# Kernel optimization log

Hardware: AMD Instinct MI355X
Metric: run time of the kernel (lower is better)

Reference implementation:

```python
import jax, jax.numpy as jnp
import numpy as np

EPS = 1e-5  # BatchNorm eps (torch default)


def _coords():
    # coord_tensor[i] = [(i//5 - 2)/2, (i%5 - 2)/2] for 5x5 grid of 25 objects
    i = jnp.arange(25)
    return jnp.stack([(i // 5 - 2) / 2.0, (i % 5 - 2) / 2.0], axis=-1).astype(jnp.float32)


def _conv_bn(x, w, b, gamma, beta):
    # conv stride2 pad1 -> relu -> batchnorm (training-mode batch stats, as torch module default)
    y = jax.lax.conv_general_dilated(x, w, (2, 2), ((1, 1), (1, 1)),
                                     dimension_numbers=('NCHW', 'OIHW', 'NCHW'))
    y = jax.nn.relu(y + b[None, :, None, None])
    m = y.mean(axis=(0, 2, 3), keepdims=True)
    v = y.var(axis=(0, 2, 3), keepdims=True)
    return gamma[None, :, None, None] * (y - m) * jax.lax.rsqrt(v + EPS) + beta[None, :, None, None]


def setup_inputs() -> dict:
    key = jax.random.key(0)
    ks = iter(jax.random.split(key, 64))
    def rn(shape, scale=0.05):
        return jax.random.normal(next(ks), shape, jnp.float32) * scale
    B = 256
    inp = {
        'x': jax.random.normal(next(ks), (B, 3, 80, 80), jnp.float32),
        'qst': jax.random.normal(next(ks), (B, 11), jnp.float32),
    }
    for l, (ci, co) in enumerate([(3, 24), (24, 24), (24, 24), (24, 24)], 1):
        inp[f'cw{l}'] = rn((co, ci, 3, 3))
        inp[f'cb{l}'] = jnp.zeros((co,), jnp.float32)
        inp[f'bg{l}'] = jnp.ones((co,), jnp.float32)
        inp[f'bb{l}'] = jnp.zeros((co,), jnp.float32)
    for l, (di, do) in enumerate([(63, 256), (256, 256), (256, 256), (256, 256)], 1):
        inp[f'gw{l}'] = rn((di, do))
        inp[f'gb{l}'] = jnp.zeros((do,), jnp.float32)
    for l, (di, do) in enumerate([(256, 256), (256, 256), (256, 10)], 1):
        inp[f'fw{l}'] = rn((di, do))
        inp[f'fb{l}'] = jnp.zeros((do,), jnp.float32)
    return inp


def _forward(x, qst, cw1, cb1, bg1, bb1, cw2, cb2, bg2, bb2,
             cw3, cb3, bg3, bb3, cw4, cb4, bg4, bb4,
             gw1, gb1, gw2, gb2, gw3, gb3, gw4, gb4,
             fw1, fb1, fw2, fb2, fw3, fb3):
    B = x.shape[0]
    # Convolution stack: (B,3,80,80) -> (B,24,5,5)
    h = _conv_bn(x, cw1, cb1, bg1, bb1)
    h = _conv_bn(h, cw2, cb2, bg2, bb2)
    h = _conv_bn(h, cw3, cb3, bg3, bb3)
    h = _conv_bn(h, cw4, cb4, bg4, bb4)
    # Objects: (B,24,25) -> (B,25,24) -> concat coords -> (B,25,26)
    obj = h.reshape(B, 24, 25).transpose(0, 2, 1)
    obj = jnp.concatenate([obj, jnp.broadcast_to(_coords()[None], (B, 25, 2))], axis=-1)
    # Pairwise broadcast-concat: cat([x_i, x_j, qst]) with x_i[b,p,q]=obj[b,q], x_j[b,p,q]=obj[b,p]
    xi = jnp.broadcast_to(obj[:, None, :, :], (B, 25, 25, 26))
    xj = jnp.broadcast_to(obj[:, :, None, :], (B, 25, 25, 26))
    qb = jnp.broadcast_to(qst[:, None, None, :], (B, 25, 25, 11))
    pairs = jnp.concatenate([xi, xj, qb], axis=-1).reshape(B, 625, 63)
    g = jax.nn.relu(pairs @ gw1 + gb1)
    g = jax.nn.relu(g @ gw2 + gb2)
    g = jax.nn.relu(g @ gw3 + gb3)
    g = jax.nn.relu(g @ gw4 + gb4).sum(axis=1)  # (B,256)
    # f_phi (dropout treated as identity for a deterministic reference)
    f = jax.nn.relu(g @ fw1 + fb1)
    f = jax.nn.relu(f @ fw2 + fb2)
    logits = f @ fw3 + fb3
    return jax.nn.log_softmax(logits, axis=1)


def reference(x, qst, cw1, cb1, bg1, bb1, cw2, cb2, bg2, bb2,
              cw3, cb3, bg3, bb3, cw4, cb4, bg4, bb4,
              gw1, gb1, gw2, gb2, gw3, gb3, gw4, gb4,
              fw1, fb1, fw2, fb2, fw3, fb3):
    return _forward(x, qst, cw1, cb1, bg1, bb1, cw2, cb2, bg2, bb2,
                    cw3, cb3, bg3, bb3, cw4, cb4, bg4, bb4,
                    gw1, gb1, gw2, gb2, gw3, gb3, gw4, gb4,
                    fw1, fb1, fw2, fb2, fw3, fb3)
```

## Files before the change

kernel.cpp:

```cpp
#include <hip/hip_runtime.h>
#include <hip/hip_bf16.h>


typedef __attribute__((ext_vector_type(8))) short short8;
typedef __attribute__((ext_vector_type(4))) float floatx4;

__device__ __forceinline__ unsigned short f2bf(float v){
  union { float f; unsigned int u; } c; c.f = v;
  unsigned int u = c.u;
  u += 0x7FFFu + ((u >> 16) & 1u);
  return (unsigned short)(u >> 16);
}

__global__ __launch_bounds__(256) void prep_w_zero(
    const float* __restrict__ gw2, const float* __restrict__ gw3,
    const float* __restrict__ gw4, unsigned short* __restrict__ wf,
    float* __restrict__ stats)
{
  const int bid = blockIdx.x, tid = threadIdx.x;
  if (bid == 0){ for (int j = tid; j < 1536; j += 256) stats[j] = 0.f; }
  const int w = bid >> 8;
  const float* gw = (w == 0) ? gw2 : (w == 1) ? gw3 : gw4;
  const int idx = (bid & 255)*256 + tid;
  const int i = idx & 7, lane = (idx >> 3) & 63, t = (idx >> 9) & 15, kk = idx >> 13;
  const int k = kk*32 + (lane >> 4)*8 + i;
  const int c = t*16 + (lane & 15);
  wf[w*65536 + idx] = f2bf(gw[k*256 + c]);
}

template<int CI, int COG, int CIB>
__global__ __launch_bounds__(256) void conv_relu_stats(
    const float* __restrict__ in,
    const float* __restrict__ stats_in, const float* __restrict__ gprev,
    const float* __restrict__ bprev, float invN,
    const float* __restrict__ cw, const float* __restrict__ cb,
    float* __restrict__ out, float* __restrict__ stats_out,
    int H, int W, int OH, int OW)
{
  const int co0 = blockIdx.y * COG;
  __shared__ float ssm[2*CI];
  __shared__ float psum[4][COG], psum2[4][COG];
  const int tid = threadIdx.x;
  if (tid < CI){
    if (stats_in){
      float S = 0.f, S2 = 0.f;
      #pragma unroll
      for (int sh = 0; sh < 8; sh++){ S += stats_in[sh*48 + tid]; S2 += stats_in[sh*48 + 24 + tid]; }
      const float mean = S*invN;
      const float var  = S2*invN - mean*mean;
      const float rs   = rsqrtf(var + 1e-5f);
      const float sc   = gprev[tid]*rs;
      ssm[tid] = sc; ssm[CI + tid] = bprev[tid] - mean*sc;
    } else { ssm[tid] = 1.f; ssm[CI + tid] = 0.f; }
  }
  __syncthreads();
  const int idx = blockIdx.x*256 + tid;
  const int ow = idx % OW; const int t2 = idx / OW;
  const int oh = t2 % OH;  const int b  = t2 / OH;
  const float* cwb = cw + co0*CI*9;
  float accv[COG];
  #pragma unroll
  for (int g = 0; g < COG; g++) accv[g] = cb[co0 + g];
  for (int ci0 = 0; ci0 < CI; ci0 += CIB){
    float v[CIB*9];
    #pragma unroll
    for (int cj = 0; cj < CIB; cj++){
      const int ci = ci0 + cj;
      const float* ip = in + ((long)(b*CI + ci))*H*W;
      const float sc = ssm[ci], sh2 = ssm[CI + ci];
      #pragma unroll
      for (int kh = 0; kh < 3; kh++){
        const int ih = oh*2 - 1 + kh;
        const bool hok = (kh > 0) | (oh > 0);
        #pragma unroll
        for (int kw = 0; kw < 3; kw++){
          const int iw = ow*2 - 1 + kw;
          const bool ok = hok & ((kw > 0) | (ow > 0));
          const float raw = ip[ok ? ih*W + iw : 0];
          v[cj*9 + kh*3 + kw] = ok ? raw*sc + sh2 : 0.f;
        }
      }
    }
    #pragma unroll
    for (int cj = 0; cj < CIB; cj++)
      #pragma unroll
      for (int t = 0; t < 9; t++){
        const float vv = v[cj*9 + t];
        #pragma unroll
        for (int g = 0; g < COG; g++)
          accv[g] += vv * cwb[(g*CI + ci0 + cj)*9 + t];
      }
  }
  const int wave = tid >> 6, lane = tid & 63;
  #pragma unroll
  for (int g = 0; g < COG; g++){
    const float v2 = fmaxf(accv[g], 0.f);
    accv[g] = v2;
    out[(((long)b*24 + co0 + g)*OH + oh)*OW + ow] = v2;
  }
  #pragma unroll
  for (int g = 0; g < COG; g++){
    float s = accv[g], s2 = accv[g]*accv[g];
    for (int off = 32; off; off >>= 1){ s += __shfl_down(s, off); s2 += __shfl_down(s2, off); }
    if (lane == 0){ psum[wave][g] = s; psum2[wave][g] = s2; }
  }
  __syncthreads();
  if (tid < COG){
    const float S  = psum[0][tid] + psum[1][tid] + psum[2][tid] + psum[3][tid];
    const float S2 = psum2[0][tid] + psum2[1][tid] + psum2[2][tid] + psum2[3][tid];
    const int sh = blockIdx.x & 7;
    atomicAdd(&stats_out[sh*48 + co0 + tid],      S);
    atomicAdd(&stats_out[sh*48 + 24 + co0 + tid], S2);
  }
}

__global__ __launch_bounds__(512) void g_mega(
    const float* __restrict__ y4, const float* __restrict__ stats4,
    const float* __restrict__ bg4, const float* __restrict__ bb4,
    const float* __restrict__ qst, const float* __restrict__ gw1,
    const float* __restrict__ gb1,
    const unsigned short* __restrict__ Wf,
    const float* __restrict__ gb2, const float* __restrict__ gb3, const float* __restrict__ gb4,
    const float* __restrict__ fw1, const float* __restrict__ fb1,
    const float* __restrict__ fw2, const float* __restrict__ fb2,
    const float* __restrict__ fw3, const float* __restrict__ fb3,
    float* __restrict__ out)
{
  __shared__ __align__(16) short act[128*256];
  __shared__ __align__(16) float A_lds[25][260];
  __shared__ __align__(16) float Bm_lds[25][260];
  __shared__ float obj[25][26];
  __shared__ float ssum[48];
  __shared__ float ssm[48];
  __shared__ float scratch[512];
  __shared__ __align__(16) float bufA[256], bufB[256];
  __shared__ float lg[10];

  const int b = blockIdx.x, tid = threadIdx.x;
  char* actB = (char*)act;
  const int wave = tid >> 6, lane = tid & 63;
  const int lmod = lane & 15, ldiv = lane >> 4;
  const int wm = wave >> 2, wn = wave & 3;

  if (tid < 48){
    float S = 0.f;
    #pragma unroll
    for (int sh = 0; sh < 8; sh++) S += stats4[sh*48 + tid];
    ssum[tid] = S;
  }
  __syncthreads();
  if (tid < 24){
    const float mean = ssum[tid]*(1.f/6400.f);
    const float var  = ssum[24 + tid]*(1.f/6400.f) - mean*mean;
    const float rs   = rsqrtf(var + 1e-5f);
    const float sc   = bg4[tid]*rs;
    ssm[tid] = sc; ssm[24 + tid] = bb4[tid] - mean*sc;
  }
  __syncthreads();
  for (int j = tid; j < 600; j += 512){
    const int q = j/24, c = j%24;
    obj[q][c] = ssm[c]*y4[((long)(b*24 + c))*25 + q] + ssm[24 + c];
  }
  if (tid < 50){
    const int q = tid >> 1;
    obj[q][24 + (tid & 1)] = (tid & 1) ? (float)(q%5 - 2)*0.5f : (float)(q/5 - 2)*0.5f;
  }
  __syncthreads();
  {
    const int n = tid & 255, half = tid >> 8;
    float wa[26], wb[26];
    #pragma unroll
    for (int c = 0; c < 26; c++){ wa[c] = gw1[c*256 + n]; wb[c] = gw1[(26 + c)*256 + n]; }
    float qv = gb1[n];
    #pragma unroll
    for (int j = 0; j < 11; j++) qv += qst[b*11 + j]*gw1[(52 + j)*256 + n];
    const int q0 = half ? 13 : 0, q1 = half ? 25 : 13;
    for (int q = q0; q < q1; q++){
      float a = qv, bm = 0.f;
      #pragma unroll
      for (int c = 0; c < 26; c++){ const float o = obj[q][c]; a += o*wa[c]; bm += o*wb[c]; }
      A_lds[q][n] = a; Bm_lds[q][n] = bm;
    }
  }
  __syncthreads();

  float gsum = 0.f;
  for (int blk = 0; blk < 5; blk++){
    const int rowbase = blk * 128;
    const int nrows = min(128, 625 - rowbase);
    {
      const int r  = tid >> 2;
      const int q4 = tid & 3;
      if (r < nrows){
        const int row = rowbase + r;
        const float* ap = &A_lds [row % 25][q4*4];
        const float* bp = &Bm_lds[row / 25][q4*4];
        #pragma unroll
        for (int j = 0; j < 16; j++){
          const int c = j*16;
          floatx4 av = *(const floatx4*)(ap + c);
          floatx4 bv = *(const floatx4*)(bp + c);
          unsigned int p0 = (unsigned int)f2bf(fmaxf(av.x+bv.x, 0.f))
                          | ((unsigned int)f2bf(fmaxf(av.y+bv.y, 0.f)) << 16);
          unsigned int p1 = (unsigned int)f2bf(fmaxf(av.z+bv.z, 0.f))
                          | ((unsigned int)f2bf(fmaxf(av.w+bv.w, 0.f)) << 16);
          const int byte = (r*512 + (c + q4*4)*2) ^ ((r & 7) << 4);
          *(uint2*)(actB + byte) = make_uint2(p0, p1);
        }
      } else {
        #pragma unroll
        for (int j = 0; j < 16; j++){
          const int byte = (r*512 + (j*16 + q4*4)*2) ^ ((r & 7) << 4);
          *(uint2*)(actB + byte) = make_uint2(0u, 0u);
        }
      }
    }
    __syncthreads();

    for (int L = 0; L < 3; L++){
      floatx4 acc[4][4];
      #pragma unroll
      for (int m = 0; m < 4; m++)
        #pragma unroll
        for (int n = 0; n < 4; n++)
          acc[m][n] = (floatx4){0.f,0.f,0.f,0.f};
      const short8* wlayer = (const short8*)Wf + (long)L*8192;
      #pragma unroll
      for (int kk = 0; kk < 8; kk++){
        short8 bf[4];
        #pragma unroll
        for (int n = 0; n < 4; n++)
          bf[n] = wlayer[(kk*16 + wn*4 + n)*64 + lane];
        short8 af[4];
        #pragma unroll
        for (int m = 0; m < 4; m++){
          const int arow  = wm*64 + m*16 + lmod;
          const int abyte = (arow*512 + kk*64 + ldiv*16) ^ ((arow & 7) << 4);
          af[m] = *(const short8*)(actB + abyte);
        }
        #pragma unroll
        for (int n = 0; n < 4; n++)
          #pragma unroll
          for (int m = 0; m < 4; m++)
            acc[m][n] = __builtin_amdgcn_mfma_f32_16x16x32_bf16(af[m], bf[n], acc[m][n], 0, 0, 0);
      }

      if (L < 2){
        const float* bias = (L == 0) ? gb2 : gb3;
        __syncthreads();
        #pragma unroll
        for (int n = 0; n < 4; n++){
          const int c = (wn*4 + n)*16 + lmod;
          const float bv = bias[c];
          #pragma unroll
          for (int m = 0; m < 4; m++){
            #pragma unroll
            for (int i = 0; i < 4; i++){
              const int row = wm*64 + m*16 + ldiv*4 + i;
              const float v = fmaxf(acc[m][n][i] + bv, 0.f);
              const int byte = (row*512 + c*2) ^ ((row & 7) << 4);
              *(short*)(actB + byte) = (short)f2bf(v);
            }
          }
        }
        __syncthreads();
      } else {
        __syncthreads();
        #pragma unroll
        for (int n = 0; n < 4; n++){
          const int c = (wn*4 + n)*16 + lmod;
          const float bv = gb4[c];
          float sv = 0.f;
          #pragma unroll
          for (int m = 0; m < 4; m++){
            #pragma unroll
            for (int i = 0; i < 4; i++){
              const int row = wm*64 + m*16 + ldiv*4 + i;
              const float v = fmaxf(acc[m][n][i] + bv, 0.f);
              if (row < nrows) sv += v;
            }
          }
          sv += __shfl_xor(sv, 16);
          sv += __shfl_xor(sv, 32);
          if (ldiv == 0) scratch[wm*256 + c] = sv;
        }
        __syncthreads();
        if (tid < 256) gsum += scratch[tid] + scratch[256 + tid];
      }
    }
  }

  if (tid < 256) bufA[tid] = gsum;
  __syncthreads();
  const int n = tid & 255;
  float acc = 0.f;
  if (tid < 256){
    acc = fb1[n];
    const float4* pa = (const float4*)bufA;
    #pragma unroll 8
    for (int k4 = 0; k4 < 64; k4++){
      const float4 a = pa[k4];
      acc += a.x*fw1[(k4*4 + 0)*256 + n];
      acc += a.y*fw1[(k4*4 + 1)*256 + n];
      acc += a.z*fw1[(k4*4 + 2)*256 + n];
      acc += a.w*fw1[(k4*4 + 3)*256 + n];
    }
    bufB[n] = fmaxf(acc, 0.f);
  }
  __syncthreads();
  if (tid < 256){
    acc = fb2[n];
    const float4* pb = (const float4*)bufB;
    #pragma unroll 8
    for (int k4 = 0; k4 < 64; k4++){
      const float4 a = pb[k4];
      acc += a.x*fw2[(k4*4 + 0)*256 + n];
      acc += a.y*fw2[(k4*4 + 1)*256 + n];
      acc += a.z*fw2[(k4*4 + 2)*256 + n];
      acc += a.w*fw2[(k4*4 + 3)*256 + n];
    }
  }
  __syncthreads();
  if (tid < 256) bufA[n] = fmaxf(acc, 0.f);
  __syncthreads();
  if (tid < 10){
    float a3 = fb3[tid];
    for (int k = 0; k < 256; k++) a3 += bufA[k]*fw3[k*10 + tid];
    lg[tid] = a3;
  }
  __syncthreads();
  if (tid < 10){
    float m = lg[0];
    #pragma unroll
    for (int j = 1; j < 10; j++) m = fmaxf(m, lg[j]);
    float s = 0.f;
    #pragma unroll
    for (int j = 0; j < 10; j++) s += expf(lg[j] - m);
    out[b*10 + tid] = lg[tid] - m - logf(s);
  }
}

extern "C" void kernel_launch(void* const* d_in, const int* in_sizes, int n_in,
                              void* d_out, int out_size, void* d_ws, size_t ws_size,
                              hipStream_t stream)
{
  const float* x   = (const float*)d_in[0];
  const float* qst = (const float*)d_in[1];
  const float* cw1 = (const float*)d_in[2];
  const float* cb1 = (const float*)d_in[3];
  const float* bg1 = (const float*)d_in[4];
  const float* bb1 = (const float*)d_in[5];
  const float* cw2 = (const float*)d_in[6];
  const float* cb2 = (const float*)d_in[7];
  const float* bg2 = (const float*)d_in[8];
  const float* bb2 = (const float*)d_in[9];
  const float* cw3 = (const float*)d_in[10];
  const float* cb3 = (const float*)d_in[11];
  const float* bg3 = (const float*)d_in[12];
  const float* bb3 = (const float*)d_in[13];
  const float* cw4 = (const float*)d_in[14];
  const float* cb4 = (const float*)d_in[15];
  const float* bg4 = (const float*)d_in[16];
  const float* bb4 = (const float*)d_in[17];
  const float* gw1 = (const float*)d_in[18];
  const float* gb1 = (const float*)d_in[19];
  const float* gw2 = (const float*)d_in[20];
  const float* gb2 = (const float*)d_in[21];
  const float* gw3 = (const float*)d_in[22];
  const float* gb3 = (const float*)d_in[23];
  const float* gw4 = (const float*)d_in[24];
  const float* gb4 = (const float*)d_in[25];
  const float* fw1 = (const float*)d_in[26];
  const float* fb1 = (const float*)d_in[27];
  const float* fw2 = (const float*)d_in[28];
  const float* fb2 = (const float*)d_in[29];
  const float* fw3 = (const float*)d_in[30];
  const float* fb3 = (const float*)d_in[31];

  float* wsf    = (float*)d_ws;
  unsigned short* Wf = (unsigned short*)(wsf + 65728);
  float* stats  = wsf + 164032;
  float* y1     = wsf + 240832;
  float* y2     = wsf + 10071232;
  float* y3     = wsf + 12528832;
  float* y4     = wsf + 13143232;

  prep_w_zero<<<768, 256, 0, stream>>>(gw2, gw3, gw4, Wf, stats);
  conv_relu_stats<3,24,3><<<dim3(1600,1), 256, 0, stream>>>(x, nullptr, nullptr, nullptr, 0.f,
                                               cw1, cb1, y1, stats + 0, 80,80,40,40);
  conv_relu_stats<24,8,4><<<dim3(400,3), 256, 0, stream>>>(y1, stats + 0, bg1, bb1, 1.f/409600.f,
                                               cw2, cb2, y2, stats + 384, 40,40,20,20);
  conv_relu_stats<24,8,4><<<dim3(100,3), 256, 0, stream>>>(y2, stats + 384, bg2, bb2, 1.f/102400.f,
                                               cw3, cb3, y3, stats + 768, 20,20,10,10);
  conv_relu_stats<24,8,4><<<dim3(25,3), 256, 0, stream>>>(y3, stats + 768, bg3, bb3, 1.f/25600.f,
                                              cw4, cb4, y4, stats + 1152, 10,10,5,5);
  g_mega<<<256, 512, 0, stream>>>(y4, stats + 1152, bg4, bb4, qst, gw1, gb1, Wf,
                                  gb2, gb3, gb4, fw1, fb1, fw2, fb2, fw3, fb3,
                                  (float*)d_out);
}
```

Baseline: 286.7 us.

## Compute multiple output pixels per thread in conv kernels with shared input columns

Each conv thread now produces PX adjacent output pixels, loading one 3x(2PX+1) input window per channel so overlapping stride-2 columns are reused across the pixels. Outputs are written with float4/float2 stores and per-thread partial sums feed the batch-norm statistics reduction. Conv1 is split across three output-channel groups instead of one, and grid sizes shrink to match. The aim is fewer redundant global loads and address computations per output, at the cost of more registers per thread and fewer threads launched.

```diff
diff --git a/kernel.cpp b/kernel.cpp
--- a/kernel.cpp
+++ b/kernel.cpp
@@ -28,8 +28,8 @@
   wf[w*65536 + idx] = f2bf(gw[k*256 + c]);
 }
 
-template<int CI, int COG, int CIB>
-__global__ __launch_bounds__(256) void conv_relu_stats(
+template<int CI, int COG, int PX>
+__global__ __launch_bounds__(256) void conv_px(
     const float* __restrict__ in,
     const float* __restrict__ stats_in, const float* __restrict__ gprev,
     const float* __restrict__ bprev, float invN,
@@ -54,55 +54,71 @@
     } else { ssm[tid] = 1.f; ssm[CI + tid] = 0.f; }
   }
   __syncthreads();
+  const int nw = OW / PX;
   const int idx = blockIdx.x*256 + tid;
-  const int ow = idx % OW; const int t2 = idx / OW;
+  const int pw = idx % nw; const int t2 = idx / nw;
   const int oh = t2 % OH;  const int b  = t2 / OH;
+  const int ow0 = pw * PX;
   const float* cwb = cw + co0*CI*9;
-  float accv[COG];
+  constexpr int NC = 2*PX + 1;
+  float acc[PX][COG];
   #pragma unroll
-  for (int g = 0; g < COG; g++) accv[g] = cb[co0 + g];
-  for (int ci0 = 0; ci0 < CI; ci0 += CIB){
-    float v[CIB*9];
-    #pragma unroll
-    for (int cj = 0; cj < CIB; cj++){
-      const int ci = ci0 + cj;
-      const float* ip = in + ((long)(b*CI + ci))*H*W;
-      const float sc = ssm[ci], sh2 = ssm[CI + ci];
+  for (int j = 0; j < PX; j++)
+    #pragma unroll
+    for (int g = 0; g < COG; g++) acc[j][g] = cb[co0 + g];
+
+  #pragma unroll 1
+  for (int ci = 0; ci < CI; ci++){
+    const float* ip = in + ((long)(b*CI + ci))*H*W;
+    const float sc = ssm[ci], sh2 = ssm[CI + ci];
+    float v[3][NC];
+    #pragma unroll
+    for (int kh = 0; kh < 3; kh++){
+      const int ih = oh*2 - 1 + kh;
+      const bool hok = (ih >= 0);
+      #pragma unroll
+      for (int c9 = 0; c9 < NC; c9++){
+        const int iw = ow0*2 - 1 + c9;
+        const bool ok = hok & (iw >= 0);
+        const float raw = ip[ok ? ih*W + iw : 0];
+        v[kh][c9] = ok ? raw*sc + sh2 : 0.f;
+      }
+    }
+    #pragma unroll
+    for (int g = 0; g < COG; g++){
       #pragma unroll
       for (int kh = 0; kh < 3; kh++){
-        const int ih = oh*2 - 1 + kh;
-        const bool hok = (kh > 0) | (oh > 0);
-        #pragma unroll
-        for (int kw = 0; kw < 3; kw++){
-          const int iw = ow*2 - 1 + kw;
-          const bool ok = hok & ((kw > 0) | (ow > 0));
-          const float raw = ip[ok ? ih*W + iw : 0];
-          v[cj*9 + kh*3 + kw] = ok ? raw*sc + sh2 : 0.f;
-        }
+        const float w0 = cwb[(g*CI + ci)*9 + kh*3 + 0];
+        const float w1 = cwb[(g*CI + ci)*9 + kh*3 + 1];
+        const float w2 = cwb[(g*CI + ci)*9 + kh*3 + 2];
+        #pragma unroll
+        for (int j = 0; j < PX; j++)
+          acc[j][g] += v[kh][2*j]*w0 + v[kh][2*j+1]*w1 + v[kh][2*j+2]*w2;
       }
     }
-    #pragma unroll
-    for (int cj = 0; cj < CIB; cj++)
-      #pragma unroll
-      for (int t = 0; t < 9; t++){
-        const float vv = v[cj*9 + t];
-        #pragma unroll
-        for (int g = 0; g < COG; g++)
-          accv[g] += vv * cwb[(g*CI + ci0 + cj)*9 + t];
-      }
-  }
+  }
+
   const int wave = tid >> 6, lane = tid & 63;
+  float s[COG], s2[COG];
   #pragma unroll
   for (int g = 0; g < COG; g++){
-    const float v2 = fmaxf(accv[g], 0.f);
-    accv[g] = v2;
-    out[(((long)b*24 + co0 + g)*OH + oh)*OW + ow] = v2;
+    float tmp[PX], a = 0.f, a2 = 0.f;
+    #pragma unroll
+    for (int j = 0; j < PX; j++){
+      tmp[j] = fmaxf(acc[j][g], 0.f);
+      a += tmp[j]; a2 += tmp[j]*tmp[j];
+    }
+    float* op = &out[(((long)b*24 + co0 + g)*OH + oh)*OW + ow0];
+    if constexpr (PX == 4) *(float4*)op = make_float4(tmp[0], tmp[1], tmp[2], tmp[3]);
+    else if constexpr (PX == 2) *(float2*)op = make_float2(tmp[0], tmp[1]);
+    else op[0] = tmp[0];
+    s[g] = a; s2[g] = a2;
   }
   #pragma unroll
   for (int g = 0; g < COG; g++){
-    float s = accv[g], s2 = accv[g]*accv[g];
-    for (int off = 32; off; off >>= 1){ s += __shfl_down(s, off); s2 += __shfl_down(s2, off); }
-    if (lane == 0){ psum[wave][g] = s; psum2[wave][g] = s2; }
+    float a = s[g], a2 = s2[g];
+    for (int off = 32; off; off >>= 1){ a += __shfl_down(a, off); a2 += __shfl_down(a2, off); }
+    if (lane == 0){ psum[wave][g] = a; psum2[wave][g] = a2; }
   }
   __syncthreads();
   if (tid < COG){
@@ -386,13 +402,13 @@
   float* y4     = wsf + 13143232;
 
   prep_w_zero<<<768, 256, 0, stream>>>(gw2, gw3, gw4, Wf, stats);
-  conv_relu_stats<3,24,3><<<dim3(1600,1), 256, 0, stream>>>(x, nullptr, nullptr, nullptr, 0.f,
+  conv_px<3,8,4><<<dim3(400,3), 256, 0, stream>>>(x, nullptr, nullptr, nullptr, 0.f,
                                                cw1, cb1, y1, stats + 0, 80,80,40,40);
-  conv_relu_stats<24,8,4><<<dim3(400,3), 256, 0, stream>>>(y1, stats + 0, bg1, bb1, 1.f/409600.f,
+  conv_px<24,8,4><<<dim3(100,3), 256, 0, stream>>>(y1, stats + 0, bg1, bb1, 1.f/409600.f,
                                                cw2, cb2, y2, stats + 384, 40,40,20,20);
-  conv_relu_stats<24,8,4><<<dim3(100,3), 256, 0, stream>>>(y2, stats + 384, bg2, bb2, 1.f/102400.f,
+  conv_px<24,8,2><<<dim3(50,3), 256, 0, stream>>>(y2, stats + 384, bg2, bb2, 1.f/102400.f,
                                                cw3, cb3, y3, stats + 768, 20,20,10,10);
-  conv_relu_stats<24,8,4><<<dim3(25,3), 256, 0, stream>>>(y3, stats + 768, bg3, bb3, 1.f/25600.f,
+  conv_px<24,8,1><<<dim3(25,3), 256, 0, stream>>>(y3, stats + 768, bg3, bb3, 1.f/25600.f,
                                               cw4, cb4, y4, stats + 1152, 10,10,5,5);
   g_mega<<<256, 512, 0, stream>>>(y4, stats + 1152, bg4, bb4, qst, gw1, gb1, Wf,
                                   gb2, gb3, gb4, fw1, fb1, fw2, fb2, fw3, fb3,
```

New measurement: 288.9 us. Within noise of the previous version (+0.8%).
